# Kernel optimization log

Measured on AMD Instinct MI355X. Metric: run time of the kernel, lower is better.

Reference implementation:

```python
import jax, jax.numpy as jnp
import numpy as np


def setup_inputs() -> dict:
    key = jax.random.key(0)
    k1, k2, k3 = jax.random.split(key, 3)
    B, Q, K, D = 4, 2048, 2048, 1024
    query = jax.random.normal(k1, (B, Q, D), dtype=jnp.float32)
    value = jax.random.normal(k2, (B, K, D), dtype=jnp.float32)
    attention_mask = jax.random.randint(k3, (B, Q, K), 0, 2, dtype=jnp.int32)
    return {"query": query, "value": value, "attention_mask": attention_mask}


def reference(query, value, attention_mask):
    # key defaults to value in the original module
    D = query.shape[-1]
    # scores[b,q,k] = sum_d (query[b,q,d] + key[b,k,d])
    #              = rowsum(query)[b,q] + rowsum(key)[b,k]  (separable outer-sum,
    # avoids the (B,Q,K,D) intermediate the torch code materializes)
    q_sum = query.sum(-1)                    # (B, Q)
    k_sum = value.sum(-1)                    # (B, K)  (key == value)
    scores = q_sum[:, :, None] + k_sum[:, None, :]   # (B, Q, K)
    scores = scores / jnp.sqrt(jnp.asarray(D, scores.dtype))  # use_scale=True
    mask_value = -1e9
    scores = scores + (1.0 - attention_mask.astype(scores.dtype)) * mask_value
    attention_weights = jax.nn.softmax(scores, axis=-1)       # (B, Q, K)
    context_vector = jnp.einsum('bqk,bkd->bqd', attention_weights, value)
    return (context_vector, attention_weights)
```

## Files before the change

kernel.cpp:

```cpp
#include <hip/hip_runtime.h>
#include <stdint.h>

#define BB 4
#define QQ 2048
#define KK 2048
#define DD 1024

__device__ inline unsigned short f2bf(float f) {
    unsigned int u = __float_as_uint(f);
    unsigned int r = (u + 0x7fffu + ((u >> 16) & 1u)) >> 16;
    return (unsigned short)r;
}

typedef short bf16x8 __attribute__((ext_vector_type(8)));
typedef float f32x4  __attribute__((ext_vector_type(4)));

__device__ inline void async16(const void* g, void* l) {
    __builtin_amdgcn_global_load_lds(
        (const __attribute__((address_space(1))) unsigned int*)g,
        (__attribute__((address_space(3))) unsigned int*)l,
        16, 0, 0);
}

__global__ __launch_bounds__(256) void transpose_conv(const float* __restrict__ V,
                                                      unsigned short* __restrict__ Vt) {
    int bid = blockIdx.x;
    int b  = bid >> 9;
    int r  = bid & 511;
    int kt = r >> 4;
    int dt = r & 15;
    int k0 = kt * 64, d0 = dt * 64;
    __shared__ float tile[64 * 65];
    int t = threadIdx.x;
    for (int i = 0; i < 4; i++) {
        int idx = i * 256 + t;
        int row = idx >> 4;
        int c4  = idx & 15;
        float4 v = *(const float4*)(V + (size_t)(b * KK + k0 + row) * DD + d0 + c4 * 4);
        float* p = &tile[row * 65 + c4 * 4];
        p[0] = v.x; p[1] = v.y; p[2] = v.z; p[3] = v.w;
    }
    __syncthreads();
    for (int i = 0; i < 4; i++) {
        int idx = i * 256 + t;
        int dr = idx >> 4;
        int kc = idx & 15;
        ushort4 o;
        o.x = f2bf(tile[(kc * 4 + 0) * 65 + dr]);
        o.y = f2bf(tile[(kc * 4 + 1) * 65 + dr]);
        o.z = f2bf(tile[(kc * 4 + 2) * 65 + dr]);
        o.w = f2bf(tile[(kc * 4 + 3) * 65 + dr]);
        *(ushort4*)(Vt + (size_t)(b * DD + d0 + dr) * KK + k0 + kc * 4) = o;
    }
}

__global__ __launch_bounds__(256) void rowsum(const float* __restrict__ V,
                                              float* __restrict__ ksum) {
    int wave = threadIdx.x >> 6, lane = threadIdx.x & 63;
    int row = blockIdx.x * 4 + wave;
    const float* p = V + (size_t)row * DD;
    float s = 0.f;
    for (int j = 0; j < 4; j++) {
        float4 v = *(const float4*)(p + j * 256 + lane * 4);
        s += v.x + v.y + v.z + v.w;
    }
    for (int off = 32; off; off >>= 1) s += __shfl_xor(s, off, 64);
    if (lane == 0) ksum[row] = s;
}

__global__ __launch_bounds__(256) void maxexp(const float* __restrict__ ksum,
                                              float* __restrict__ e) {
    int b = blockIdx.x;
    int t = threadIdx.x;
    float s[8];
    float m = -1e30f;
    for (int j = 0; j < 8; j++) {
        s[j] = ksum[b * KK + t + j * 256] * 0.03125f;
        m = fmaxf(m, s[j]);
    }
    for (int off = 32; off; off >>= 1) m = fmaxf(m, __shfl_xor(m, off, 64));
    __shared__ float red[4];
    int wave = t >> 6, lane = t & 63;
    if (lane == 0) red[wave] = m;
    __syncthreads();
    m = fmaxf(fmaxf(red[0], red[1]), fmaxf(red[2], red[3]));
    for (int j = 0; j < 8; j++) e[b * KK + t + j * 256] = __expf(s[j] - m);
}

__global__ __launch_bounds__(256) void weights_k(const int* __restrict__ mask,
                                                 const float* __restrict__ e,
                                                 float* __restrict__ wout,
                                                 unsigned short* __restrict__ wb16) {
    int row = blockIdx.x;
    int b = row >> 11;
    int t = threadIdx.x;
    const int*   mp = mask + (size_t)row * KK;
    const float* ep = e + (size_t)b * KK;
    int kA = 4 * t, kB = 1024 + 4 * t;
    int4 ma = *(const int4*)(mp + kA);
    int4 mb = *(const int4*)(mp + kB);
    float4 ea = *(const float4*)(ep + kA);
    float4 eb = *(const float4*)(ep + kB);
    float4 wa, wb;
    wa.x = ma.x ? ea.x : 0.f;  wa.y = ma.y ? ea.y : 0.f;
    wa.z = ma.z ? ea.z : 0.f;  wa.w = ma.w ? ea.w : 0.f;
    wb.x = mb.x ? eb.x : 0.f;  wb.y = mb.y ? eb.y : 0.f;
    wb.z = mb.z ? eb.z : 0.f;  wb.w = mb.w ? eb.w : 0.f;
    float part = (wa.x + wa.y + wa.z + wa.w) + (wb.x + wb.y + wb.z + wb.w);
    for (int off = 32; off; off >>= 1) part += __shfl_xor(part, off, 64);
    __shared__ float red[4];
    int wave = t >> 6, lane = t & 63;
    if (lane == 0) red[wave] = part;
    __syncthreads();
    float S = (red[0] + red[1]) + (red[2] + red[3]);
    float rS = 1.f / S;
    wa.x *= rS; wa.y *= rS; wa.z *= rS; wa.w *= rS;
    wb.x *= rS; wb.y *= rS; wb.z *= rS; wb.w *= rS;
    *(float4*)(wout + (size_t)row * KK + kA) = wa;
    *(float4*)(wout + (size_t)row * KK + kB) = wb;
    ushort4 pa, pb;
    pa.x = f2bf(wa.x); pa.y = f2bf(wa.y); pa.z = f2bf(wa.z); pa.w = f2bf(wa.w);
    pb.x = f2bf(wb.x); pb.y = f2bf(wb.y); pb.z = f2bf(wb.z); pb.w = f2bf(wb.w);
    *(ushort4*)(wb16 + (size_t)row * KK + kA) = pa;
    *(ushort4*)(wb16 + (size_t)row * KK + kB) = pb;
}

__global__ __launch_bounds__(256) void gemm_ctx(const unsigned short* __restrict__ Wb,
                                                const unsigned short* __restrict__ Vt,
                                                float* __restrict__ ctx) {
    int bid = blockIdx.x;
    int b  = bid >> 7;
    int r  = bid & 127;
    int qt = r >> 3, dt = r & 7;
    int q0 = qt * 128, n0 = dt * 128;
    __shared__ unsigned short As[128 * 32];
    __shared__ unsigned short Bs[128 * 32];
    int tid = threadIdx.x, wave = tid >> 6, lane = tid & 63;
    int quad = lane >> 4, lm = lane & 15;
    int wm = wave >> 1, wn = wave & 1;
    const unsigned short* Ag = Wb + (size_t)(b * QQ + q0) * KK;
    const unsigned short* Bg = Vt + (size_t)(b * DD + n0) * KK;
    int c0 = wave * 2, c1 = c0 + 1;
    int lrow = lane >> 2, lk = (lane & 3) * 8;
    const unsigned short* agp0 = Ag + (size_t)(c0 * 16 + lrow) * KK + lk;
    const unsigned short* agp1 = Ag + (size_t)(c1 * 16 + lrow) * KK + lk;
    const unsigned short* bgp0 = Bg + (size_t)(c0 * 16 + lrow) * KK + lk;
    const unsigned short* bgp1 = Bg + (size_t)(c1 * 16 + lrow) * KK + lk;
    unsigned short* lA0 = &As[c0 * 512];
    unsigned short* lA1 = &As[c1 * 512];
    unsigned short* lB0 = &Bs[c0 * 512];
    unsigned short* lB1 = &Bs[c1 * 512];

    f32x4 acc[4][4];
    for (int i = 0; i < 4; i++)
        for (int j = 0; j < 4; j++) acc[i][j] = 0.f;

    for (int k0 = 0; k0 < KK; k0 += 32) {
        if (k0) __syncthreads();
        async16(agp0 + k0, lA0);
        async16(agp1 + k0, lA1);
        async16(bgp0 + k0, lB0);
        async16(bgp1 + k0, lB1);
        __syncthreads();
        bf16x8 a[4], bv[4];
        for (int i = 0; i < 4; i++) {
            a[i]  = *(const bf16x8*)&As[(wm * 64 + i * 16 + lm) * 32 + quad * 8];
            bv[i] = *(const bf16x8*)&Bs[(wn * 64 + i * 16 + lm) * 32 + quad * 8];
        }
        for (int i = 0; i < 4; i++)
            for (int j = 0; j < 4; j++)
                acc[i][j] = __builtin_amdgcn_mfma_f32_16x16x32_bf16(a[i], bv[j], acc[i][j], 0, 0, 0);
    }
    for (int i = 0; i < 4; i++) {
        int rowb = q0 + wm * 64 + i * 16 + quad * 4;
        for (int j = 0; j < 4; j++) {
            int col = n0 + wn * 64 + j * 16 + lm;
            for (int rr = 0; rr < 4; rr++)
                ctx[(size_t)(b * QQ + rowb + rr) * DD + col] = acc[i][j][rr];
        }
    }
}

extern "C" void kernel_launch(void* const* d_in, const int* in_sizes, int n_in,
                              void* d_out, int out_size, void* d_ws, size_t ws_size,
                              hipStream_t stream) {
    const float* value = (const float*)d_in[1];
    const int*   mask  = (const int*)d_in[2];
    float* out = (float*)d_out;

    unsigned short* Vt = (unsigned short*)d_ws;
    unsigned short* Wb = Vt + (size_t)BB * DD * KK;
    float* ksum = (float*)(Wb + (size_t)BB * QQ * KK);
    float* e    = ksum + BB * KK;

    float* ctx  = out;
    float* wout = out + (size_t)BB * QQ * DD;

    transpose_conv<<<BB * 512, 256, 0, stream>>>(value, Vt);
    rowsum<<<(BB * KK) / 4, 256, 0, stream>>>(value, ksum);
    maxexp<<<BB, 256, 0, stream>>>(ksum, e);
    weights_k<<<BB * QQ, 256, 0, stream>>>(mask, e, wout, Wb);
    gemm_ctx<<<BB * 128, 256, 0, stream>>>(Wb, Vt, ctx);
}
```

Before: 256.5 us.

## Widen GEMM K-tile with XOR-swizzled LDS, drop max pass, wave-per-row weights

The context GEMM now stages 64-wide K tiles in LDS with an XOR swizzle on the 16-byte chunks. This is meant to avoid LDS bank conflicts on the MFMA operand reads and to halve the number of barrier round-trips per tile. The separate max/exp kernel is folded into the row-sum kernel, which exponentiates the scaled key sum directly without subtracting the batch maximum. That removes one launch but relies on the scores staying small enough not to overflow exp. The softmax-weights kernel now handles one row per wavefront, using only shuffle reductions instead of a block-level LDS reduction and barrier.

Result: faster. 246.5 us (-3.9%).

```diff
diff --git a/kernel.cpp b/kernel.cpp
--- a/kernel.cpp
+++ b/kernel.cpp
@@ -54,8 +54,8 @@
     }
 }
 
-__global__ __launch_bounds__(256) void rowsum(const float* __restrict__ V,
-                                              float* __restrict__ ksum) {
+__global__ __launch_bounds__(256) void rowexp(const float* __restrict__ V,
+                                              float* __restrict__ e) {
     int wave = threadIdx.x >> 6, lane = threadIdx.x & 63;
     int row = blockIdx.x * 4 + wave;
     const float* p = V + (size_t)row * DD;
@@ -65,64 +65,41 @@
         s += v.x + v.y + v.z + v.w;
     }
     for (int off = 32; off; off >>= 1) s += __shfl_xor(s, off, 64);
-    if (lane == 0) ksum[row] = s;
-}
-
-__global__ __launch_bounds__(256) void maxexp(const float* __restrict__ ksum,
-                                              float* __restrict__ e) {
-    int b = blockIdx.x;
-    int t = threadIdx.x;
-    float s[8];
-    float m = -1e30f;
-    for (int j = 0; j < 8; j++) {
-        s[j] = ksum[b * KK + t + j * 256] * 0.03125f;
-        m = fmaxf(m, s[j]);
-    }
-    for (int off = 32; off; off >>= 1) m = fmaxf(m, __shfl_xor(m, off, 64));
-    __shared__ float red[4];
-    int wave = t >> 6, lane = t & 63;
-    if (lane == 0) red[wave] = m;
-    __syncthreads();
-    m = fmaxf(fmaxf(red[0], red[1]), fmaxf(red[2], red[3]));
-    for (int j = 0; j < 8; j++) e[b * KK + t + j * 256] = __expf(s[j] - m);
+    if (lane == 0) e[row] = __expf(s * 0.03125f);
 }
 
 __global__ __launch_bounds__(256) void weights_k(const int* __restrict__ mask,
                                                  const float* __restrict__ e,
                                                  float* __restrict__ wout,
                                                  unsigned short* __restrict__ wb16) {
-    int row = blockIdx.x;
+    int wave = threadIdx.x >> 6, lane = threadIdx.x & 63;
+    int row = blockIdx.x * 4 + wave;
     int b = row >> 11;
-    int t = threadIdx.x;
-    const int*   mp = mask + (size_t)row * KK;
-    const float* ep = e + (size_t)b * KK;
-    int kA = 4 * t, kB = 1024 + 4 * t;
-    int4 ma = *(const int4*)(mp + kA);
-    int4 mb = *(const int4*)(mp + kB);
-    float4 ea = *(const float4*)(ep + kA);
-    float4 eb = *(const float4*)(ep + kB);
-    float4 wa, wb;
-    wa.x = ma.x ? ea.x : 0.f;  wa.y = ma.y ? ea.y : 0.f;
-    wa.z = ma.z ? ea.z : 0.f;  wa.w = ma.w ? ea.w : 0.f;
-    wb.x = mb.x ? eb.x : 0.f;  wb.y = mb.y ? eb.y : 0.f;
-    wb.z = mb.z ? eb.z : 0.f;  wb.w = mb.w ? eb.w : 0.f;
-    float part = (wa.x + wa.y + wa.z + wa.w) + (wb.x + wb.y + wb.z + wb.w);
-    for (int off = 32; off; off >>= 1) part += __shfl_xor(part, off, 64);
-    __shared__ float red[4];
-    int wave = t >> 6, lane = t & 63;
-    if (lane == 0) red[wave] = part;
-    __syncthreads();
-    float S = (red[0] + red[1]) + (red[2] + red[3]);
-    float rS = 1.f / S;
-    wa.x *= rS; wa.y *= rS; wa.z *= rS; wa.w *= rS;
-    wb.x *= rS; wb.y *= rS; wb.z *= rS; wb.w *= rS;
-    *(float4*)(wout + (size_t)row * KK + kA) = wa;
-    *(float4*)(wout + (size_t)row * KK + kB) = wb;
-    ushort4 pa, pb;
-    pa.x = f2bf(wa.x); pa.y = f2bf(wa.y); pa.z = f2bf(wa.z); pa.w = f2bf(wa.w);
-    pb.x = f2bf(wb.x); pb.y = f2bf(wb.y); pb.z = f2bf(wb.z); pb.w = f2bf(wb.w);
-    *(ushort4*)(wb16 + (size_t)row * KK + kA) = pa;
-    *(ushort4*)(wb16 + (size_t)row * KK + kB) = pb;
+    const int4*   mp = (const int4*)(mask + (size_t)row * KK);
+    const float4* ep = (const float4*)(e + (size_t)b * KK);
+    float4 w[8];
+    float s = 0.f;
+    for (int j = 0; j < 8; j++) {
+        int4   m  = mp[lane + j * 64];
+        float4 ev = ep[lane + j * 64];
+        w[j].x = m.x ? ev.x : 0.f;
+        w[j].y = m.y ? ev.y : 0.f;
+        w[j].z = m.z ? ev.z : 0.f;
+        w[j].w = m.w ? ev.w : 0.f;
+        s += (w[j].x + w[j].y) + (w[j].z + w[j].w);
+    }
+    for (int off = 32; off; off >>= 1) s += __shfl_xor(s, off, 64);
+    float rS = 1.f / s;
+    float4*  wp = (float4*)(wout + (size_t)row * KK);
+    ushort4* bp = (ushort4*)(wb16 + (size_t)row * KK);
+    for (int j = 0; j < 8; j++) {
+        float4 v = w[j];
+        v.x *= rS; v.y *= rS; v.z *= rS; v.w *= rS;
+        wp[lane + j * 64] = v;
+        ushort4 pk;
+        pk.x = f2bf(v.x); pk.y = f2bf(v.y); pk.z = f2bf(v.z); pk.w = f2bf(v.w);
+        bp[lane + j * 64] = pk;
+    }
 }
 
 __global__ __launch_bounds__(256) void gemm_ctx(const unsigned short* __restrict__ Wb,
@@ -133,43 +110,45 @@
     int r  = bid & 127;
     int qt = r >> 3, dt = r & 7;
     int q0 = qt * 128, n0 = dt * 128;
-    __shared__ unsigned short As[128 * 32];
-    __shared__ unsigned short Bs[128 * 32];
+    __shared__ unsigned short As[128 * 64];
+    __shared__ unsigned short Bs[128 * 64];
     int tid = threadIdx.x, wave = tid >> 6, lane = tid & 63;
     int quad = lane >> 4, lm = lane & 15;
     int wm = wave >> 1, wn = wave & 1;
-    const unsigned short* Ag = Wb + (size_t)(b * QQ + q0) * KK;
-    const unsigned short* Bg = Vt + (size_t)(b * DD + n0) * KK;
-    int c0 = wave * 2, c1 = c0 + 1;
-    int lrow = lane >> 2, lk = (lane & 3) * 8;
-    const unsigned short* agp0 = Ag + (size_t)(c0 * 16 + lrow) * KK + lk;
-    const unsigned short* agp1 = Ag + (size_t)(c1 * 16 + lrow) * KK + lk;
-    const unsigned short* bgp0 = Bg + (size_t)(c0 * 16 + lrow) * KK + lk;
-    const unsigned short* bgp1 = Bg + (size_t)(c1 * 16 + lrow) * KK + lk;
-    unsigned short* lA0 = &As[c0 * 512];
-    unsigned short* lA1 = &As[c1 * 512];
-    unsigned short* lB0 = &Bs[c0 * 512];
-    unsigned short* lB1 = &Bs[c1 * 512];
+
+    int srow   = lane >> 3;
+    int schunk = (lane & 7) ^ srow;
+    const unsigned short* Ag = Wb + (size_t)(b * QQ + q0 + wave * 8 + srow) * KK + schunk * 8;
+    const unsigned short* Bg = Vt + (size_t)(b * DD + n0 + wave * 8 + srow) * KK + schunk * 8;
+    unsigned short* lA = &As[(wave * 8) * 64];
+    unsigned short* lB = &Bs[(wave * 8) * 64];
+
+    int m7 = lm & 7;
+    int xa0 = lm * 64 + ((0 + quad) ^ m7) * 8;
+    int xa1 = lm * 64 + ((4 + quad) ^ m7) * 8;
 
     f32x4 acc[4][4];
     for (int i = 0; i < 4; i++)
         for (int j = 0; j < 4; j++) acc[i][j] = 0.f;
 
-    for (int k0 = 0; k0 < KK; k0 += 32) {
+    for (int k0 = 0; k0 < KK; k0 += 64) {
         if (k0) __syncthreads();
-        async16(agp0 + k0, lA0);
-        async16(agp1 + k0, lA1);
-        async16(bgp0 + k0, lB0);
-        async16(bgp1 + k0, lB1);
+        for (int c = 0; c < 4; c++) {
+            async16(Ag + (size_t)(c * 32) * KK + k0, lA + c * 32 * 64);
+            async16(Bg + (size_t)(c * 32) * KK + k0, lB + c * 32 * 64);
+        }
         __syncthreads();
-        bf16x8 a[4], bv[4];
+        bf16x8 a[4][2], bv[4][2];
         for (int i = 0; i < 4; i++) {
-            a[i]  = *(const bf16x8*)&As[(wm * 64 + i * 16 + lm) * 32 + quad * 8];
-            bv[i] = *(const bf16x8*)&Bs[(wn * 64 + i * 16 + lm) * 32 + quad * 8];
+            a[i][0]  = *(const bf16x8*)&As[(wm * 64 + i * 16) * 64 + xa0];
+            a[i][1]  = *(const bf16x8*)&As[(wm * 64 + i * 16) * 64 + xa1];
+            bv[i][0] = *(const bf16x8*)&Bs[(wn * 64 + i * 16) * 64 + xa0];
+            bv[i][1] = *(const bf16x8*)&Bs[(wn * 64 + i * 16) * 64 + xa1];
         }
-        for (int i = 0; i < 4; i++)
-            for (int j = 0; j < 4; j++)
-                acc[i][j] = __builtin_amdgcn_mfma_f32_16x16x32_bf16(a[i], bv[j], acc[i][j], 0, 0, 0);
+        for (int h = 0; h < 2; h++)
+            for (int i = 0; i < 4; i++)
+                for (int j = 0; j < 4; j++)
+                    acc[i][j] = __builtin_amdgcn_mfma_f32_16x16x32_bf16(a[i][h], bv[j][h], acc[i][j], 0, 0, 0);
     }
     for (int i = 0; i < 4; i++) {
         int rowb = q0 + wm * 64 + i * 16 + quad * 4;
@@ -190,15 +169,13 @@
 
     unsigned short* Vt = (unsigned short*)d_ws;
     unsigned short* Wb = Vt + (size_t)BB * DD * KK;
-    float* ksum = (float*)(Wb + (size_t)BB * QQ * KK);
-    float* e    = ksum + BB * KK;
+    float* e = (float*)(Wb + (size_t)BB * QQ * KK);
 
     float* ctx  = out;
     float* wout = out + (size_t)BB * QQ * DD;
 
+    rowexp<<<(BB * KK) / 4, 256, 0, stream>>>(value, e);
     transpose_conv<<<BB * 512, 256, 0, stream>>>(value, Vt);
-    rowsum<<<(BB * KK) / 4, 256, 0, stream>>>(value, ksum);
-    maxexp<<<BB, 256, 0, stream>>>(ksum, e);
-    weights_k<<<BB * QQ, 256, 0, stream>>>(mask, e, wout, Wb);
+    weights_k<<<(BB * QQ) / 4, 256, 0, stream>>>(mask, e, wout, Wb);
     gemm_ctx<<<BB * 128, 256, 0, stream>>>(Wb, Vt, ctx);
 }
```
